# Kernel optimization log

Hardware: AMD Instinct MI355X
Metric: run time of the kernel (lower is better)

## Reference

```python
import jax, jax.numpy as jnp
import numpy as np

N_NODES = 50000
N_EDGES = 800000
INPUT_DIM = 8
HIDDEN_DIM = 128


def setup_inputs() -> dict:
    key = jax.random.key(0)
    k = jax.random.split(key, 8)
    x = jax.random.normal(k[0], (N_NODES, INPUT_DIM), dtype=jnp.float32)
    edge_index = jax.random.randint(k[1], (2, N_EDGES), 0, N_NODES, dtype=jnp.int64)
    edge_attr = jax.random.uniform(k[2], (N_EDGES, 1), dtype=jnp.float32)
    node_embedding = jax.random.normal(k[3], (N_NODES, HIDDEN_DIM), dtype=jnp.float32)
    # Linear weights stored as [in, out] so y = x @ W (bias=False everywhere)
    s1 = 1.0 / np.sqrt(INPUT_DIM)
    sh = 1.0 / np.sqrt(HIDDEN_DIM)
    W1 = jax.random.uniform(k[4], (INPUT_DIM, HIDDEN_DIM), jnp.float32, -s1, s1)
    W2 = jax.random.uniform(k[5], (HIDDEN_DIM, HIDDEN_DIM), jnp.float32, -sh, sh)
    W3 = jax.random.uniform(k[6], (HIDDEN_DIM, HIDDEN_DIM), jnp.float32, -sh, sh)
    W4 = jax.random.uniform(k[7], (1, HIDDEN_DIM), jnp.float32, -1.0, 1.0)
    return {"x": x, "edge_index": edge_index, "edge_attr": edge_attr,
            "node_embedding": node_embedding, "W1": W1, "W2": W2, "W3": W3, "W4": W4}


def reference(x, edge_index, edge_attr, node_embedding, W1, W2, W3, W4):
    n = x.shape[0]
    row, col = edge_index[0], edge_index[1]
    # theta_1(x): [N, hidden]
    node_feature_embedding = x @ W1
    # gather neighbor embeddings along edges, scatter-sum to destination rows
    node_embedding_aggr = jax.ops.segment_sum(node_embedding[col], row, num_segments=n)
    # relu(theta_4(edge_attr)): [E, hidden], then scatter-sum to rows
    edge_feature_embedding = jax.nn.relu(edge_attr @ W4)
    edge_embedding_aggr = jax.ops.segment_sum(edge_feature_embedding, row, num_segments=n)
    return jax.nn.relu(node_feature_embedding + node_embedding_aggr @ W2 + edge_embedding_aggr @ W3)
```

## Files before the change

### kernel.cpp

```cpp
#include <hip/hip_runtime.h>

#define N_NODES 50000
#define N_EDGES 800000
#define IN_DIM  8
#define HD      128
#define N_SCAN_BLOCKS ((N_NODES + 255) / 256)
#define NREP 16
#define NTILES ((N_NODES + 63) / 64)
#define N_HIST_BLOCKS (N_EDGES / 256)
#define GRID_P1 (NTILES * 5)

typedef unsigned short ushort_t;
typedef unsigned int uint_t;
typedef __attribute__((ext_vector_type(8))) short short8;
typedef __attribute__((ext_vector_type(4))) float float4v;

static __device__ inline unsigned short f2bf(float f) {
    unsigned u = __float_as_uint(f);
    unsigned r = (u + 0x7FFF + ((u >> 16) & 1)) >> 16;
    return (unsigned short)r;
}
static __device__ inline float bf2f(unsigned short b) {
    return __uint_as_float(((unsigned)b) << 16);
}

__global__ void prep_kernel(const float* __restrict__ W2,
                            short8* __restrict__ blob) {
    int t = threadIdx.x;
#pragma unroll
    for (int i = 0; i < 8; ++i) {
        int slot = t * 8 + i;
        int f    = slot >> 6;
        int lane = slot & 63;
        int ct = f >> 2, ki = f & 3;
        int n16 = lane & 15, quad = lane >> 4;
        short8 fr;
#pragma unroll
        for (int j = 0; j < 8; ++j) {
            int k = ki * 32 + quad * 8 + j;
            fr[j] = (short)f2bf(W2[k * HD + ct * 16 + n16]);
        }
        blob[slot] = fr;
    }
}

__global__ __launch_bounds__(256, 2)
void phase1_kernel(const float* __restrict__ emb,
                   const short8* __restrict__ blob,
                   ushort_t* __restrict__ T16,
                   const int* __restrict__ ei,
                   int* __restrict__ cnt,
                   ushort_t* __restrict__ rank16) {
    __shared__ short8 sblob[2048];
    int sel = blockIdx.x % 5;

    if (sel != 0) {
        int c = (blockIdx.x / 5) * 4 + sel - 1;
        if (c >= N_HIST_BLOCKS) return;
        int e = c * 256 + threadIdx.x;
        int rep = c & (NREP - 1);
        int r = ei[e];
        int rank = atomicAdd(&cnt[rep * N_NODES + r], 1);
        rank16[e] = (ushort_t)rank;
        return;
    }

    int tt   = blockIdx.x / 5;
    int t    = threadIdx.x;
    int wave = t >> 6;
    int lane = t & 63;
    int n16  = lane & 15;
    int quad = lane >> 4;

#pragma unroll
    for (int i = 0; i < 8; ++i)
        sblob[t * 8 + i] = blob[t * 8 + i];
    __syncthreads();

    short8 bfrag[8][4];
#pragma unroll
    for (int ct = 0; ct < 8; ++ct)
#pragma unroll
        for (int ki = 0; ki < 4; ++ki)
            bfrag[ct][ki] = sblob[(ct * 4 + ki) * 64 + lane];

    int rowbase = tt * 64 + wave * 16;
    int row  = rowbase + n16;
    int rowc = row < N_NODES ? row : N_NODES - 1;
    const float4* arow = (const float4*)(emb + (size_t)rowc * HD);

    short8 afrag[4];
#pragma unroll
    for (int ki = 0; ki < 4; ++ki) {
        float4 lo = arow[ki * 8 + quad * 2];
        float4 hi = arow[ki * 8 + quad * 2 + 1];
        short8 a;
        a[0] = (short)f2bf(lo.x); a[1] = (short)f2bf(lo.y);
        a[2] = (short)f2bf(lo.z); a[3] = (short)f2bf(lo.w);
        a[4] = (short)f2bf(hi.x); a[5] = (short)f2bf(hi.y);
        a[6] = (short)f2bf(hi.z); a[7] = (short)f2bf(hi.w);
        afrag[ki] = a;
    }

    float4v acc[8];
#pragma unroll
    for (int ct = 0; ct < 8; ++ct) acc[ct] = (float4v){0.f, 0.f, 0.f, 0.f};

#pragma unroll
    for (int ki = 0; ki < 4; ++ki)
#pragma unroll
        for (int ct = 0; ct < 8; ++ct)
            acc[ct] = __builtin_amdgcn_mfma_f32_16x16x32_bf16(
                afrag[ki], bfrag[ct][ki], acc[ct], 0, 0, 0);

#pragma unroll
    for (int reg = 0; reg < 4; ++reg) {
        int r = rowbase + quad * 4 + reg;
        if (r < N_NODES) {
#pragma unroll
            for (int ct = 0; ct < 8; ++ct)
                T16[(size_t)r * HD + ct * 16 + n16] = f2bf(acc[ct][reg]);
        }
    }
}

__global__ void scan1_kernel(const int* __restrict__ cnt,
                             int* __restrict__ off,
                             int* __restrict__ bases,
                             int* __restrict__ blocksums) {
    __shared__ int lds[256];
    int t = threadIdx.x;
    int n = blockIdx.x * 256 + t;
    int c[NREP];
    int tsum = 0;
#pragma unroll
    for (int r = 0; r < NREP; ++r) {
        c[r] = (n < N_NODES) ? cnt[r * N_NODES + n] : 0;
        tsum += c[r];
    }
    lds[t] = tsum;
    __syncthreads();
    for (int o = 1; o < 256; o <<= 1) {
        int add = (t >= o) ? lds[t - o] : 0;
        __syncthreads();
        lds[t] += add;
        __syncthreads();
    }
    int ex = lds[t] - tsum;
    if (n < N_NODES) {
        off[n] = ex;
        int run = ex;
#pragma unroll
        for (int r = 0; r < NREP; ++r) {
            bases[r * N_NODES + n] = run;
            run += c[r];
        }
    }
    if (t == 255) blocksums[blockIdx.x] = lds[255];
}

__global__ void scan2_v3_kernel(int* __restrict__ blocksums,
                                const float* __restrict__ W4,
                                const float* __restrict__ W3,
                                float* __restrict__ v3) {
    int t = threadIdx.x;
    if (blockIdx.x == 1) {
        if (t < HD) {
            float acc = 0.f;
            for (int k = 0; k < HD; ++k) {
                float w = W4[k];
                w = w > 0.f ? w : 0.f;
                acc += w * W3[k * HD + t];
            }
            v3[t] = acc;
        }
        return;
    }
    __shared__ int lds[256];
    int v = (t < N_SCAN_BLOCKS) ? blocksums[t] : 0;
    lds[t] = v;
    __syncthreads();
    for (int o = 1; o < 256; o <<= 1) {
        int add = (t >= o) ? lds[t - o] : 0;
        __syncthreads();
        lds[t] += add;
        __syncthreads();
    }
    if (t < N_SCAN_BLOCKS) blocksums[t] = lds[t] - v;
}

__global__ void fill_kernel(const int* __restrict__ ei,
                            const float* __restrict__ attr,
                            const ushort_t* __restrict__ rank16,
                            const int* __restrict__ bases,
                            const int* __restrict__ bsums,
                            uint_t* __restrict__ packed) {
    int e = blockIdx.x * 256 + threadIdx.x;
    int rep = (e >> 8) & (NREP - 1);
    int r = ei[e];
    int pos = bases[rep * N_NODES + r] + bsums[r >> 8] + (int)rank16[e];
    uint_t p = ((uint_t)f2bf(attr[e]) << 16) | (uint_t)ei[N_EDGES + e];
    packed[pos] = p;
}

__global__ void aggregate_kernel(const int* __restrict__ off,
                                 const int* __restrict__ bsums,
                                 const uint_t* __restrict__ packed,
                                 const ushort_t* __restrict__ T16,
                                 const float* __restrict__ x,
                                 const float* __restrict__ W1,
                                 const float* __restrict__ v3,
                                 float* __restrict__ out) {
    int tid  = blockIdx.x * 256 + threadIdx.x;
    int node = tid >> 4;
    int lane = tid & 15;
    int s  = off[node] + bsums[node >> 8];
    int e1 = (node + 1 == N_NODES) ? N_EDGES
                                   : off[node + 1] + bsums[(node + 1) >> 8];
    int deg = e1 - s;

    float acc[8];
#pragma unroll
    for (int i = 0; i < 8; ++i) acc[i] = 0.f;
    float ssum = 0.f;

    for (int base = 0; base < deg; base += 16) {
        int rem = deg - base; if (rem > 16) rem = 16;
        uint_t p = 0;
        if (lane < rem) p = packed[s + base + lane];
        ssum += __uint_as_float(p & 0xFFFF0000u);
        int col = (int)(p & 0xFFFFu);
        int j = 0;
        for (; j + 4 <= rem; j += 4) {
            int c0 = __shfl(col, j + 0, 16);
            int c1 = __shfl(col, j + 1, 16);
            int c2 = __shfl(col, j + 2, 16);
            int c3 = __shfl(col, j + 3, 16);
            short8 t0 = ((const short8*)(T16 + (size_t)c0 * HD))[lane];
            short8 t1 = ((const short8*)(T16 + (size_t)c1 * HD))[lane];
            short8 t2 = ((const short8*)(T16 + (size_t)c2 * HD))[lane];
            short8 t3 = ((const short8*)(T16 + (size_t)c3 * HD))[lane];
#pragma unroll
            for (int i = 0; i < 8; ++i)
                acc[i] += (bf2f((ushort_t)t0[i]) + bf2f((ushort_t)t1[i]))
                        + (bf2f((ushort_t)t2[i]) + bf2f((ushort_t)t3[i]));
        }
        for (; j < rem; ++j) {
            int c = __shfl(col, j, 16);
            short8 tv = ((const short8*)(T16 + (size_t)c * HD))[lane];
#pragma unroll
            for (int i = 0; i < 8; ++i)
                acc[i] += bf2f((ushort_t)tv[i]);
        }
    }
    for (int o = 8; o; o >>= 1) ssum += __shfl_xor(ssum, o, 16);

    const float4* v3p = (const float4*)v3;
    float4 b0 = v3p[lane * 2], b1 = v3p[lane * 2 + 1];
    acc[0] += ssum * b0.x; acc[1] += ssum * b0.y;
    acc[2] += ssum * b0.z; acc[3] += ssum * b0.w;
    acc[4] += ssum * b1.x; acc[5] += ssum * b1.y;
    acc[6] += ssum * b1.z; acc[7] += ssum * b1.w;
#pragma unroll
    for (int i = 0; i < IN_DIM; ++i) {
        float xi = x[node * IN_DIM + i];
        const float4* wp = (const float4*)(W1 + i * HD);
        float4 w0 = wp[lane * 2], w1 = wp[lane * 2 + 1];
        acc[0] += xi * w0.x; acc[1] += xi * w0.y;
        acc[2] += xi * w0.z; acc[3] += xi * w0.w;
        acc[4] += xi * w1.x; acc[5] += xi * w1.y;
        acc[6] += xi * w1.z; acc[7] += xi * w1.w;
    }
    float4 o0, o1;
    o0.x = fmaxf(acc[0], 0.f); o0.y = fmaxf(acc[1], 0.f);
    o0.z = fmaxf(acc[2], 0.f); o0.w = fmaxf(acc[3], 0.f);
    o1.x = fmaxf(acc[4], 0.f); o1.y = fmaxf(acc[5], 0.f);
    o1.z = fmaxf(acc[6], 0.f); o1.w = fmaxf(acc[7], 0.f);
    float4* op = (float4*)(out + (size_t)node * HD);
    op[lane * 2]     = o0;
    op[lane * 2 + 1] = o1;
}

extern "C" void kernel_launch(void* const* d_in, const int* in_sizes, int n_in,
                              void* d_out, int out_size, void* d_ws, size_t ws_size,
                              hipStream_t stream) {
    const float* x    = (const float*)d_in[0];
    const int*   ei   = (const int*)  d_in[1];
    const float* attr = (const float*)d_in[2];
    const float* emb  = (const float*)d_in[3];
    const float* W1   = (const float*)d_in[4];
    const float* W2   = (const float*)d_in[5];
    const float* W3   = (const float*)d_in[6];
    const float* W4   = (const float*)d_in[7];
    float* out = (float*)d_out;

    char* w = (char*)d_ws;
    uint_t*   packed = (uint_t*)w;
    ushort_t* T16    = (ushort_t*)(w + (size_t)N_EDGES * 4);
    short8*   blob   = (short8*)((char*)T16 + (size_t)N_NODES * HD * 2);
    int*      off    = (int*)((char*)blob + 2048 * 16);
    int*      bases  = off + N_NODES + 4;
    int*      cnt    = bases + NREP * N_NODES;
    int*      bsums  = cnt + NREP * N_NODES;
    float*    v3     = (float*)(bsums + 256);
    ushort_t* rank16 = (ushort_t*)(v3 + HD);

    hipMemsetAsync(cnt, 0, (size_t)NREP * N_NODES * sizeof(int), stream);

    prep_kernel  <<<1, 256, 0, stream>>>(W2, blob);
    phase1_kernel<<<GRID_P1, 256, 0, stream>>>(emb, blob, T16, ei, cnt, rank16);
    scan1_kernel <<<N_SCAN_BLOCKS, 256, 0, stream>>>(cnt, off, bases, bsums);
    scan2_v3_kernel<<<2, 256, 0, stream>>>(bsums, W4, W3, v3);
    fill_kernel  <<<N_HIST_BLOCKS, 256, 0, stream>>>(ei, attr, rank16, bases, bsums, packed);
    aggregate_kernel<<<(N_NODES * 16) / 256, 256, 0, stream>>>(
        off, bsums, packed, T16, x, W1, v3, out);
}
```

Measured before the change: 188.6 us.

## Fuse preprocessing kernels into persistent mega-kernel with software grid barriers

Replaces the prep, phase1, scan1, scan2 and fill kernels with one persistent kernel of 512 blocks that strides over tiles and edges and separates phases with atomic-counter grid barriers. Each block now converts W2 to bf16 fragments itself, so the separate prep kernel and its blob buffer go away, and the barrier counter is zeroed by the existing memset. The aim is to remove several kernel launch gaps and tail effects. It relies on all 512 blocks being co-resident, since the spin barrier deadlocks otherwise. The aggregate gather loop is also unrolled from 4 to 8 neighbor loads to get more memory requests in flight.

Result: slower. 328.1 us (+74.0%).

```diff
diff --git a/kernel.cpp b/kernel.cpp
--- a/kernel.cpp
+++ b/kernel.cpp
@@ -8,7 +8,7 @@
 #define NREP 16
 #define NTILES ((N_NODES + 63) / 64)
 #define N_HIST_BLOCKS (N_EDGES / 256)
-#define GRID_P1 (NTILES * 5)
+#define GRID 512
 
 typedef unsigned short ushort_t;
 typedef unsigned int uint_t;
@@ -24,183 +24,182 @@
     return __uint_as_float(((unsigned)b) << 16);
 }
 
-__global__ void prep_kernel(const float* __restrict__ W2,
-                            short8* __restrict__ blob) {
-    int t = threadIdx.x;
+static __device__ inline void grid_barrier(int* bar, int phase) {
+    __syncthreads();
+    if (threadIdx.x == 0) {
+        __threadfence();
+        atomicAdd(bar, 1);
+        int target = GRID * (phase + 1);
+        while (atomicAdd(bar, 0) < target)
+            __builtin_amdgcn_s_sleep(8);
+        __threadfence();
+    }
+    __syncthreads();
+}
+
+__global__ __launch_bounds__(256, 2)
+void mega_kernel(const float* __restrict__ emb,
+                 const float* __restrict__ W2,
+                 const float* __restrict__ W3,
+                 const float* __restrict__ W4,
+                 const int* __restrict__ ei,
+                 const float* __restrict__ attr,
+                 ushort_t* __restrict__ T16,
+                 int* __restrict__ cnt,
+                 ushort_t* __restrict__ rank16,
+                 int* __restrict__ off,
+                 int* __restrict__ bases,
+                 int* __restrict__ bsums,
+                 float* __restrict__ v3,
+                 uint_t* __restrict__ packed,
+                 int* __restrict__ bar) {
+    __shared__ int smem_i[8192];
+    short8* sblob = (short8*)smem_i;
+
+    int t    = threadIdx.x;
+    int b    = blockIdx.x;
+    int wave = t >> 6;
+    int lane = t & 63;
+    int n16  = lane & 15;
+    int quad = lane >> 4;
+
 #pragma unroll
     for (int i = 0; i < 8; ++i) {
-        int slot = t * 8 + i;
-        int f    = slot >> 6;
-        int lane = slot & 63;
+        int f  = wave * 8 + i;
         int ct = f >> 2, ki = f & 3;
-        int n16 = lane & 15, quad = lane >> 4;
         short8 fr;
 #pragma unroll
         for (int j = 0; j < 8; ++j) {
             int k = ki * 32 + quad * 8 + j;
             fr[j] = (short)f2bf(W2[k * HD + ct * 16 + n16]);
         }
-        blob[slot] = fr;
-    }
-}
-
-__global__ __launch_bounds__(256, 2)
-void phase1_kernel(const float* __restrict__ emb,
-                   const short8* __restrict__ blob,
-                   ushort_t* __restrict__ T16,
-                   const int* __restrict__ ei,
-                   int* __restrict__ cnt,
-                   ushort_t* __restrict__ rank16) {
-    __shared__ short8 sblob[2048];
-    int sel = blockIdx.x % 5;
-
-    if (sel != 0) {
-        int c = (blockIdx.x / 5) * 4 + sel - 1;
-        if (c >= N_HIST_BLOCKS) return;
-        int e = c * 256 + threadIdx.x;
+        sblob[f * 64 + lane] = fr;
+    }
+    __syncthreads();
+
+    short8 bfrag[8][4];
+#pragma unroll
+    for (int ct = 0; ct < 8; ++ct)
+#pragma unroll
+        for (int ki = 0; ki < 4; ++ki)
+            bfrag[ct][ki] = sblob[(ct * 4 + ki) * 64 + lane];
+
+    for (int tt = b; tt < NTILES; tt += GRID) {
+        int rowbase = tt * 64 + wave * 16;
+        int row  = rowbase + n16;
+        int rowc = row < N_NODES ? row : N_NODES - 1;
+        const float4* arow = (const float4*)(emb + (size_t)rowc * HD);
+
+        short8 afrag[4];
+#pragma unroll
+        for (int ki = 0; ki < 4; ++ki) {
+            float4 lo = arow[ki * 8 + quad * 2];
+            float4 hi = arow[ki * 8 + quad * 2 + 1];
+            short8 a;
+            a[0] = (short)f2bf(lo.x); a[1] = (short)f2bf(lo.y);
+            a[2] = (short)f2bf(lo.z); a[3] = (short)f2bf(lo.w);
+            a[4] = (short)f2bf(hi.x); a[5] = (short)f2bf(hi.y);
+            a[6] = (short)f2bf(hi.z); a[7] = (short)f2bf(hi.w);
+            afrag[ki] = a;
+        }
+
+        float4v acc[8];
+#pragma unroll
+        for (int ct = 0; ct < 8; ++ct) acc[ct] = (float4v){0.f, 0.f, 0.f, 0.f};
+
+#pragma unroll
+        for (int ki = 0; ki < 4; ++ki)
+#pragma unroll
+            for (int ct = 0; ct < 8; ++ct)
+                acc[ct] = __builtin_amdgcn_mfma_f32_16x16x32_bf16(
+                    afrag[ki], bfrag[ct][ki], acc[ct], 0, 0, 0);
+
+#pragma unroll
+        for (int reg = 0; reg < 4; ++reg) {
+            int r = rowbase + quad * 4 + reg;
+            if (r < N_NODES) {
+#pragma unroll
+                for (int ct = 0; ct < 8; ++ct)
+                    T16[(size_t)r * HD + ct * 16 + n16] = f2bf(acc[ct][reg]);
+            }
+        }
+    }
+
+    for (int c = b; c < N_HIST_BLOCKS; c += GRID) {
+        int e = c * 256 + t;
         int rep = c & (NREP - 1);
         int r = ei[e];
         int rank = atomicAdd(&cnt[rep * N_NODES + r], 1);
         rank16[e] = (ushort_t)rank;
-        return;
-    }
-
-    int tt   = blockIdx.x / 5;
-    int t    = threadIdx.x;
-    int wave = t >> 6;
-    int lane = t & 63;
-    int n16  = lane & 15;
-    int quad = lane >> 4;
-
-#pragma unroll
-    for (int i = 0; i < 8; ++i)
-        sblob[t * 8 + i] = blob[t * 8 + i];
-    __syncthreads();
-
-    short8 bfrag[8][4];
-#pragma unroll
-    for (int ct = 0; ct < 8; ++ct)
-#pragma unroll
-        for (int ki = 0; ki < 4; ++ki)
-            bfrag[ct][ki] = sblob[(ct * 4 + ki) * 64 + lane];
-
-    int rowbase = tt * 64 + wave * 16;
-    int row  = rowbase + n16;
-    int rowc = row < N_NODES ? row : N_NODES - 1;
-    const float4* arow = (const float4*)(emb + (size_t)rowc * HD);
-
-    short8 afrag[4];
-#pragma unroll
-    for (int ki = 0; ki < 4; ++ki) {
-        float4 lo = arow[ki * 8 + quad * 2];
-        float4 hi = arow[ki * 8 + quad * 2 + 1];
-        short8 a;
-        a[0] = (short)f2bf(lo.x); a[1] = (short)f2bf(lo.y);
-        a[2] = (short)f2bf(lo.z); a[3] = (short)f2bf(lo.w);
-        a[4] = (short)f2bf(hi.x); a[5] = (short)f2bf(hi.y);
-        a[6] = (short)f2bf(hi.z); a[7] = (short)f2bf(hi.w);
-        afrag[ki] = a;
-    }
-
-    float4v acc[8];
-#pragma unroll
-    for (int ct = 0; ct < 8; ++ct) acc[ct] = (float4v){0.f, 0.f, 0.f, 0.f};
-
-#pragma unroll
-    for (int ki = 0; ki < 4; ++ki)
-#pragma unroll
-        for (int ct = 0; ct < 8; ++ct)
-            acc[ct] = __builtin_amdgcn_mfma_f32_16x16x32_bf16(
-                afrag[ki], bfrag[ct][ki], acc[ct], 0, 0, 0);
-
-#pragma unroll
-    for (int reg = 0; reg < 4; ++reg) {
-        int r = rowbase + quad * 4 + reg;
-        if (r < N_NODES) {
-#pragma unroll
-            for (int ct = 0; ct < 8; ++ct)
-                T16[(size_t)r * HD + ct * 16 + n16] = f2bf(acc[ct][reg]);
-        }
-    }
-}
-
-__global__ void scan1_kernel(const int* __restrict__ cnt,
-                             int* __restrict__ off,
-                             int* __restrict__ bases,
-                             int* __restrict__ blocksums) {
-    __shared__ int lds[256];
-    int t = threadIdx.x;
-    int n = blockIdx.x * 256 + t;
-    int c[NREP];
-    int tsum = 0;
-#pragma unroll
-    for (int r = 0; r < NREP; ++r) {
-        c[r] = (n < N_NODES) ? cnt[r * N_NODES + n] : 0;
-        tsum += c[r];
-    }
-    lds[t] = tsum;
-    __syncthreads();
-    for (int o = 1; o < 256; o <<= 1) {
-        int add = (t >= o) ? lds[t - o] : 0;
+    }
+
+    if (b == 300 && t < HD) {
+        float acc = 0.f;
+        for (int k = 0; k < HD; ++k) {
+            float w = W4[k];
+            w = w > 0.f ? w : 0.f;
+            acc += w * W3[k * HD + t];
+        }
+        v3[t] = acc;
+    }
+
+    grid_barrier(bar, 0);
+
+    if (b < N_SCAN_BLOCKS) {
+        int n = b * 256 + t;
+        int c[NREP];
+        int tsum = 0;
+#pragma unroll
+        for (int r = 0; r < NREP; ++r) {
+            c[r] = (n < N_NODES) ? cnt[r * N_NODES + n] : 0;
+            tsum += c[r];
+        }
+        smem_i[t] = tsum;
         __syncthreads();
-        lds[t] += add;
+        for (int o = 1; o < 256; o <<= 1) {
+            int add = (t >= o) ? smem_i[t - o] : 0;
+            __syncthreads();
+            smem_i[t] += add;
+            __syncthreads();
+        }
+        int ex = smem_i[t] - tsum;
+        if (n < N_NODES) {
+            off[n] = ex;
+            int run = ex;
+#pragma unroll
+            for (int r = 0; r < NREP; ++r) {
+                bases[r * N_NODES + n] = run;
+                run += c[r];
+            }
+        }
+        if (t == 255) bsums[b] = smem_i[255];
+    }
+
+    grid_barrier(bar, 1);
+
+    if (b == 0) {
+        int v = (t < N_SCAN_BLOCKS) ? bsums[t] : 0;
+        smem_i[t] = v;
         __syncthreads();
-    }
-    int ex = lds[t] - tsum;
-    if (n < N_NODES) {
-        off[n] = ex;
-        int run = ex;
-#pragma unroll
-        for (int r = 0; r < NREP; ++r) {
-            bases[r * N_NODES + n] = run;
-            run += c[r];
-        }
-    }
-    if (t == 255) blocksums[blockIdx.x] = lds[255];
-}
-
-__global__ void scan2_v3_kernel(int* __restrict__ blocksums,
-                                const float* __restrict__ W4,
-                                const float* __restrict__ W3,
-                                float* __restrict__ v3) {
-    int t = threadIdx.x;
-    if (blockIdx.x == 1) {
-        if (t < HD) {
-            float acc = 0.f;
-            for (int k = 0; k < HD; ++k) {
-                float w = W4[k];
-                w = w > 0.f ? w : 0.f;
-                acc += w * W3[k * HD + t];
-            }
-            v3[t] = acc;
-        }
-        return;
-    }
-    __shared__ int lds[256];
-    int v = (t < N_SCAN_BLOCKS) ? blocksums[t] : 0;
-    lds[t] = v;
-    __syncthreads();
-    for (int o = 1; o < 256; o <<= 1) {
-        int add = (t >= o) ? lds[t - o] : 0;
-        __syncthreads();
-        lds[t] += add;
-        __syncthreads();
-    }
-    if (t < N_SCAN_BLOCKS) blocksums[t] = lds[t] - v;
-}
-
-__global__ void fill_kernel(const int* __restrict__ ei,
-                            const float* __restrict__ attr,
-                            const ushort_t* __restrict__ rank16,
-                            const int* __restrict__ bases,
-                            const int* __restrict__ bsums,
-                            uint_t* __restrict__ packed) {
-    int e = blockIdx.x * 256 + threadIdx.x;
-    int rep = (e >> 8) & (NREP - 1);
-    int r = ei[e];
-    int pos = bases[rep * N_NODES + r] + bsums[r >> 8] + (int)rank16[e];
-    uint_t p = ((uint_t)f2bf(attr[e]) << 16) | (uint_t)ei[N_EDGES + e];
-    packed[pos] = p;
+        for (int o = 1; o < 256; o <<= 1) {
+            int add = (t >= o) ? smem_i[t - o] : 0;
+            __syncthreads();
+            smem_i[t] += add;
+            __syncthreads();
+        }
+        if (t < N_SCAN_BLOCKS) bsums[t] = smem_i[t] - v;
+    }
+
+    grid_barrier(bar, 2);
+
+    for (int c = b; c < N_HIST_BLOCKS; c += GRID) {
+        int e = c * 256 + t;
+        int rep = c & (NREP - 1);
+        int r = ei[e];
+        int pos = bases[rep * N_NODES + r] + bsums[r >> 8] + (int)rank16[e];
+        uint_t p = ((uint_t)f2bf(attr[e]) << 16) | (uint_t)ei[N_EDGES + e];
+        packed[pos] = p;
+    }
 }
 
 __global__ void aggregate_kernel(const int* __restrict__ off,
@@ -231,19 +230,19 @@
         ssum += __uint_as_float(p & 0xFFFF0000u);
         int col = (int)(p & 0xFFFFu);
         int j = 0;
-        for (; j + 4 <= rem; j += 4) {
-            int c0 = __shfl(col, j + 0, 16);
-            int c1 = __shfl(col, j + 1, 16);
-            int c2 = __shfl(col, j + 2, 16);
-            int c3 = __shfl(col, j + 3, 16);
-            short8 t0 = ((const short8*)(T16 + (size_t)c0 * HD))[lane];
-            short8 t1 = ((const short8*)(T16 + (size_t)c1 * HD))[lane];
-            short8 t2 = ((const short8*)(T16 + (size_t)c2 * HD))[lane];
-            short8 t3 = ((const short8*)(T16 + (size_t)c3 * HD))[lane];
+        for (; j + 8 <= rem; j += 8) {
+            short8 tv[8];
+#pragma unroll
+            for (int q = 0; q < 8; ++q) {
+                int c = __shfl(col, j + q, 16);
+                tv[q] = ((const short8*)(T16 + (size_t)c * HD))[lane];
+            }
 #pragma unroll
             for (int i = 0; i < 8; ++i)
-                acc[i] += (bf2f((ushort_t)t0[i]) + bf2f((ushort_t)t1[i]))
-                        + (bf2f((ushort_t)t2[i]) + bf2f((ushort_t)t3[i]));
+                acc[i] += ((bf2f((ushort_t)tv[0][i]) + bf2f((ushort_t)tv[1][i]))
+                         + (bf2f((ushort_t)tv[2][i]) + bf2f((ushort_t)tv[3][i])))
+                        + ((bf2f((ushort_t)tv[4][i]) + bf2f((ushort_t)tv[5][i]))
+                         + (bf2f((ushort_t)tv[6][i]) + bf2f((ushort_t)tv[7][i])));
         }
         for (; j < rem; ++j) {
             int c = __shfl(col, j, 16);
@@ -297,21 +296,19 @@
     char* w = (char*)d_ws;
     uint_t*   packed = (uint_t*)w;
     ushort_t* T16    = (ushort_t*)(w + (size_t)N_EDGES * 4);
-    short8*   blob   = (short8*)((char*)T16 + (size_t)N_NODES * HD * 2);
-    int*      off    = (int*)((char*)blob + 2048 * 16);
+    int*      off    = (int*)((char*)T16 + (size_t)N_NODES * HD * 2);
     int*      bases  = off + N_NODES + 4;
     int*      cnt    = bases + NREP * N_NODES;
-    int*      bsums  = cnt + NREP * N_NODES;
+    int*      bar    = cnt + NREP * N_NODES;
+    int*      bsums  = bar + 16;
     float*    v3     = (float*)(bsums + 256);
     ushort_t* rank16 = (ushort_t*)(v3 + HD);
 
-    hipMemsetAsync(cnt, 0, (size_t)NREP * N_NODES * sizeof(int), stream);
-
-    prep_kernel  <<<1, 256, 0, stream>>>(W2, blob);
-    phase1_kernel<<<GRID_P1, 256, 0, stream>>>(emb, blob, T16, ei, cnt, rank16);
-    scan1_kernel <<<N_SCAN_BLOCKS, 256, 0, stream>>>(cnt, off, bases, bsums);
-    scan2_v3_kernel<<<2, 256, 0, stream>>>(bsums, W4, W3, v3);
-    fill_kernel  <<<N_HIST_BLOCKS, 256, 0, stream>>>(ei, attr, rank16, bases, bsums, packed);
+    hipMemsetAsync(cnt, 0, (size_t)NREP * N_NODES * sizeof(int) + 16 * sizeof(int), stream);
+
+    mega_kernel<<<GRID, 256, 0, stream>>>(emb, W2, W3, W4, ei, attr,
+                                          T16, cnt, rank16, off, bases,
+                                          bsums, v3, packed, bar);
     aggregate_kernel<<<(N_NODES * 16) / 256, 256, 0, stream>>>(
         off, bsums, packed, T16, x, W1, v3, out);
 }
```

## Merge scan passes via last-block atomic counter and unroll gather loop by eight

Applied to the files above, without the earlier changes.

Merges the two scan kernels into one launch. The last block to finish, detected with an atomic done counter, performs the block-sum scan, and an extra block computes v3. This removes one kernel launch and the gap between launches. The aggregate gather loop also now issues eight row loads per iteration instead of four, to raise memory-level parallelism, at some cost in register use. The done counter is zeroed by extending the existing memset.

Result: slower. 199.7 us (+5.9%).

```diff
diff --git a/kernel.cpp b/kernel.cpp
--- a/kernel.cpp
+++ b/kernel.cpp
@@ -124,47 +124,20 @@
     }
 }
 
-__global__ void scan1_kernel(const int* __restrict__ cnt,
-                             int* __restrict__ off,
-                             int* __restrict__ bases,
-                             int* __restrict__ blocksums) {
+__global__ void scan_kernel(const int* __restrict__ cnt,
+                            int* __restrict__ off,
+                            int* __restrict__ bases,
+                            int* __restrict__ bsums,
+                            int* __restrict__ done,
+                            const float* __restrict__ W4,
+                            const float* __restrict__ W3,
+                            float* __restrict__ v3) {
     __shared__ int lds[256];
+    __shared__ int is_last;
     int t = threadIdx.x;
-    int n = blockIdx.x * 256 + t;
-    int c[NREP];
-    int tsum = 0;
-#pragma unroll
-    for (int r = 0; r < NREP; ++r) {
-        c[r] = (n < N_NODES) ? cnt[r * N_NODES + n] : 0;
-        tsum += c[r];
-    }
-    lds[t] = tsum;
-    __syncthreads();
-    for (int o = 1; o < 256; o <<= 1) {
-        int add = (t >= o) ? lds[t - o] : 0;
-        __syncthreads();
-        lds[t] += add;
-        __syncthreads();
-    }
-    int ex = lds[t] - tsum;
-    if (n < N_NODES) {
-        off[n] = ex;
-        int run = ex;
-#pragma unroll
-        for (int r = 0; r < NREP; ++r) {
-            bases[r * N_NODES + n] = run;
-            run += c[r];
-        }
-    }
-    if (t == 255) blocksums[blockIdx.x] = lds[255];
-}
-
-__global__ void scan2_v3_kernel(int* __restrict__ blocksums,
-                                const float* __restrict__ W4,
-                                const float* __restrict__ W3,
-                                float* __restrict__ v3) {
-    int t = threadIdx.x;
-    if (blockIdx.x == 1) {
+    int b = blockIdx.x;
+
+    if (b == N_SCAN_BLOCKS) {
         if (t < HD) {
             float acc = 0.f;
             for (int k = 0; k < HD; ++k) {
@@ -176,9 +149,16 @@
         }
         return;
     }
-    __shared__ int lds[256];
-    int v = (t < N_SCAN_BLOCKS) ? blocksums[t] : 0;
-    lds[t] = v;
+
+    int n = b * 256 + t;
+    int c[NREP];
+    int tsum = 0;
+#pragma unroll
+    for (int r = 0; r < NREP; ++r) {
+        c[r] = (n < N_NODES) ? cnt[r * N_NODES + n] : 0;
+        tsum += c[r];
+    }
+    lds[t] = tsum;
     __syncthreads();
     for (int o = 1; o < 256; o <<= 1) {
         int add = (t >= o) ? lds[t - o] : 0;
@@ -186,7 +166,43 @@
         lds[t] += add;
         __syncthreads();
     }
-    if (t < N_SCAN_BLOCKS) blocksums[t] = lds[t] - v;
+    int ex = lds[t] - tsum;
+    if (n < N_NODES) {
+        off[n] = ex;
+        int run = ex;
+#pragma unroll
+        for (int r = 0; r < NREP; ++r) {
+            bases[r * N_NODES + n] = run;
+            run += c[r];
+        }
+    }
+    if (t == 255)
+        __hip_atomic_store(&bsums[b], lds[255], __ATOMIC_RELEASE,
+                           __HIP_MEMORY_SCOPE_AGENT);
+    __syncthreads();
+
+    if (t == 0) {
+        int prev = __hip_atomic_fetch_add(done, 1, __ATOMIC_ACQ_REL,
+                                          __HIP_MEMORY_SCOPE_AGENT);
+        is_last = (prev == N_SCAN_BLOCKS - 1);
+    }
+    __syncthreads();
+    if (!is_last) return;
+
+    int v = (t < N_SCAN_BLOCKS)
+          ? __hip_atomic_load(&bsums[t], __ATOMIC_ACQUIRE,
+                              __HIP_MEMORY_SCOPE_AGENT)
+          : 0;
+    __syncthreads();
+    lds[t] = v;
+    __syncthreads();
+    for (int o = 1; o < 256; o <<= 1) {
+        int add = (t >= o) ? lds[t - o] : 0;
+        __syncthreads();
+        lds[t] += add;
+        __syncthreads();
+    }
+    if (t < N_SCAN_BLOCKS) bsums[t] = lds[t] - v;
 }
 
 __global__ void fill_kernel(const int* __restrict__ ei,
@@ -231,19 +247,19 @@
         ssum += __uint_as_float(p & 0xFFFF0000u);
         int col = (int)(p & 0xFFFFu);
         int j = 0;
-        for (; j + 4 <= rem; j += 4) {
-            int c0 = __shfl(col, j + 0, 16);
-            int c1 = __shfl(col, j + 1, 16);
-            int c2 = __shfl(col, j + 2, 16);
-            int c3 = __shfl(col, j + 3, 16);
-            short8 t0 = ((const short8*)(T16 + (size_t)c0 * HD))[lane];
-            short8 t1 = ((const short8*)(T16 + (size_t)c1 * HD))[lane];
-            short8 t2 = ((const short8*)(T16 + (size_t)c2 * HD))[lane];
-            short8 t3 = ((const short8*)(T16 + (size_t)c3 * HD))[lane];
+        for (; j + 8 <= rem; j += 8) {
+            short8 tv[8];
+#pragma unroll
+            for (int q = 0; q < 8; ++q) {
+                int c = __shfl(col, j + q, 16);
+                tv[q] = ((const short8*)(T16 + (size_t)c * HD))[lane];
+            }
 #pragma unroll
             for (int i = 0; i < 8; ++i)
-                acc[i] += (bf2f((ushort_t)t0[i]) + bf2f((ushort_t)t1[i]))
-                        + (bf2f((ushort_t)t2[i]) + bf2f((ushort_t)t3[i]));
+                acc[i] += ((bf2f((ushort_t)tv[0][i]) + bf2f((ushort_t)tv[1][i]))
+                         + (bf2f((ushort_t)tv[2][i]) + bf2f((ushort_t)tv[3][i])))
+                        + ((bf2f((ushort_t)tv[4][i]) + bf2f((ushort_t)tv[5][i]))
+                         + (bf2f((ushort_t)tv[6][i]) + bf2f((ushort_t)tv[7][i])));
         }
         for (; j < rem; ++j) {
             int c = __shfl(col, j, 16);
@@ -301,16 +317,17 @@
     int*      off    = (int*)((char*)blob + 2048 * 16);
     int*      bases  = off + N_NODES + 4;
     int*      cnt    = bases + NREP * N_NODES;
-    int*      bsums  = cnt + NREP * N_NODES;
+    int*      done   = cnt + NREP * N_NODES;
+    int*      bsums  = done + 16;
     float*    v3     = (float*)(bsums + 256);
     ushort_t* rank16 = (ushort_t*)(v3 + HD);
 
-    hipMemsetAsync(cnt, 0, (size_t)NREP * N_NODES * sizeof(int), stream);
+    hipMemsetAsync(cnt, 0, (size_t)NREP * N_NODES * sizeof(int) + 16 * sizeof(int), stream);
 
     prep_kernel  <<<1, 256, 0, stream>>>(W2, blob);
     phase1_kernel<<<GRID_P1, 256, 0, stream>>>(emb, blob, T16, ei, cnt, rank16);
-    scan1_kernel <<<N_SCAN_BLOCKS, 256, 0, stream>>>(cnt, off, bases, bsums);
-    scan2_v3_kernel<<<2, 256, 0, stream>>>(bsums, W4, W3, v3);
+    scan_kernel  <<<N_SCAN_BLOCKS + 1, 256, 0, stream>>>(cnt, off, bases, bsums,
+                                                         done, W4, W3, v3);
     fill_kernel  <<<N_HIST_BLOCKS, 256, 0, stream>>>(ei, attr, rank16, bases, bsums, packed);
     aggregate_kernel<<<(N_NODES * 16) / 256, 256, 0, stream>>>(
         off, bsums, packed, T16, x, W1, v3, out);
```
